# Performance work log

Measured on AMD Instinct MI355X. Metric: run time of the kernel, lower is better.

The kernel has to match this reference:

```python
import jax, jax.numpy as jnp
import numpy as np

N_BINS = 10  # init default of ECELoss


def setup_inputs() -> dict:
    key = jax.random.key(0)
    k1, k2 = jax.random.split(key)
    N, C = 2_000_000, 100
    raw = jax.random.normal(k1, (N, C), dtype=jnp.float32)
    # module computes exp(logits) and expects confidences in (0, 1],
    # so the logits it receives are log-probabilities
    logits = jax.nn.log_softmax(raw, axis=1)
    labels = jax.random.randint(k2, (N,), 0, C, dtype=jnp.int64)
    return {"logits": logits, "labels": labels}


def reference(logits, labels):
    softmaxes = jnp.exp(logits)                       # [N, C]
    confidences = jnp.max(softmaxes, axis=1)          # [N]
    predictions = jnp.argmax(softmaxes, axis=1)       # [N]
    accuracies = (predictions == labels).astype(jnp.float32)

    n = confidences.shape[0]
    # bin i holds conf in (i/n_bins, (i+1)/n_bins]  ->  ceil(conf*n_bins)-1
    bin_idx = jnp.ceil(confidences * N_BINS).astype(jnp.int32) - 1
    # conf <= 0 belongs to no bin (strict lower bound on bin 0); conf > 1
    # already maps to an out-of-range index. Out-of-range ids are dropped
    # by segment_sum.
    bin_idx = jnp.where(confidences <= 0.0, N_BINS, bin_idx)

    ones = jnp.ones_like(confidences)
    counts = jax.ops.segment_sum(ones, bin_idx, num_segments=N_BINS)
    sum_conf = jax.ops.segment_sum(confidences, bin_idx, num_segments=N_BINS)
    sum_acc = jax.ops.segment_sum(accuracies, bin_idx, num_segments=N_BINS)

    prop_in_bin = counts / n
    safe = jnp.maximum(counts, 1.0)
    gap = jnp.abs(sum_conf / safe - sum_acc / safe)
    ece = jnp.sum(jnp.where(counts > 0, gap * prop_in_bin, 0.0))
    return ece.reshape(1)
```

## Files before the change

kernel.cpp:

```cpp
#include <hip/hip_runtime.h>
#include <math.h>

#define NBINS 10
#define MAIN_BLOCKS 2048
#define MAIN_THREADS 256


__global__ void ece_zero_ws(float* ws) {
    int i = threadIdx.x;
    if (i < 3 * NBINS) ws[i] = 0.0f;
}

__global__ __launch_bounds__(MAIN_THREADS) void ece_main(
        const float* __restrict__ logits,
        const int* __restrict__ labels,
        float* __restrict__ ws,
        int N) {
    __shared__ float sbin[3 * NBINS];
    const int tid = threadIdx.x;
    if (tid < 3 * NBINS) sbin[tid] = 0.0f;
    __syncthreads();

    const int lane = tid & 63;
    const int waveInBlock = tid >> 6;
    const int wavesPerBlock = MAIN_THREADS >> 6;
    const long long globalWave = (long long)blockIdx.x * wavesPerBlock + waveInBlock;
    const long long totalWaves = (long long)gridDim.x * wavesPerBlock;

    const int half = lane >> 5;
    const int hlane = lane & 31;

    const long long nPairs = ((long long)N + 1) >> 1;
    const float4* logits4 = (const float4*)logits;

    for (long long p = globalWave; p < nPairs; p += totalWaves) {
        const long long row = 2 * p + half;
        const bool rowValid = (row < (long long)N);

        float m = -INFINITY;
        int midx = 0;
        if (rowValid && hlane < 25) {
            float4 v = logits4[row * 25 + hlane];
            const int e = hlane * 4;
            m = v.x; midx = e;
            if (v.y > m) { m = v.y; midx = e + 1; }
            if (v.z > m) { m = v.z; midx = e + 2; }
            if (v.w > m) { m = v.w; midx = e + 3; }
        }

        #pragma unroll
        for (int off = 16; off >= 1; off >>= 1) {
            float om = __shfl_xor(m, off, 32);
            int   oi = __shfl_xor(midx, off, 32);
            if (om > m || (om == m && oi < midx)) { m = om; midx = oi; }
        }

        if (rowValid && hlane == 0) {
            const float conf = expf(m);
            const int b = (int)ceilf(conf * 10.0f) - 1;
            const float acc = (midx == labels[row]) ? 1.0f : 0.0f;
            if (b >= 0 && b < NBINS) {
                atomicAdd(&sbin[b], 1.0f);
                atomicAdd(&sbin[NBINS + b], conf);
                atomicAdd(&sbin[2 * NBINS + b], acc);
            }
        }
    }

    __syncthreads();
    if (tid < 3 * NBINS) {
        const float v = sbin[tid];
        if (v != 0.0f) atomicAdd(&ws[tid], v);
    }
}

__global__ void ece_final(const float* __restrict__ ws, float* __restrict__ out, int N) {
    if (threadIdx.x == 0 && blockIdx.x == 0) {
        float ece = 0.0f;
        for (int b = 0; b < NBINS; ++b) {
            const float cnt = ws[b];
            if (cnt > 0.0f) {
                const float avg_conf = ws[NBINS + b] / cnt;
                const float avg_acc  = ws[2 * NBINS + b] / cnt;
                ece += fabsf(avg_conf - avg_acc) * (cnt / (float)N);
            }
        }
        out[0] = ece;
    }
}

extern "C" void kernel_launch(void* const* d_in, const int* in_sizes, int n_in,
                              void* d_out, int out_size, void* d_ws, size_t ws_size,
                              hipStream_t stream) {
    const float* logits = (const float*)d_in[0];
    const int*   labels = (const int*)d_in[1];
    float* out = (float*)d_out;
    float* ws  = (float*)d_ws;

    const int N = in_sizes[1];

    ece_zero_ws<<<1, 64, 0, stream>>>(ws);
    ece_main<<<MAIN_BLOCKS, MAIN_THREADS, 0, stream>>>(logits, labels, ws, N);
    ece_final<<<1, 64, 0, stream>>>(ws, out, N);
}
```

Before: 1.040 ms.

## Switch to one thread per row with a full register-held row scan

Each thread now loads an entire 100-float row as 25 float4 values into registers and runs a sequential argmax, replacing the scheme where half-waves split a row and reduced it with shuffles. This removes the shuffle reduction and the idle lanes, and gives each thread many independent loads in flight. The cost is uncoalesced access: adjacent threads read addresses 400 bytes apart. It also uses far more registers, which lowers occupancy, and shared-memory atomics now come from every thread at once and may contend.

```diff
diff --git a/kernel.cpp b/kernel.cpp
--- a/kernel.cpp
+++ b/kernel.cpp
@@ -4,6 +4,7 @@
 #define NBINS 10
 #define MAIN_BLOCKS 2048
 #define MAIN_THREADS 256
+#define NV4 25
 
 
 __global__ void ece_zero_ws(float* ws) {
@@ -21,56 +22,42 @@
     if (tid < 3 * NBINS) sbin[tid] = 0.0f;
     __syncthreads();
 
-    const int lane = tid & 63;
-    const int waveInBlock = tid >> 6;
-    const int wavesPerBlock = MAIN_THREADS >> 6;
-    const long long globalWave = (long long)blockIdx.x * wavesPerBlock + waveInBlock;
-    const long long totalWaves = (long long)gridDim.x * wavesPerBlock;
+    const float4* __restrict__ lg4 = (const float4*)logits;
+    const long long stride = (long long)gridDim.x * MAIN_THREADS;
+    long long row = (long long)blockIdx.x * MAIN_THREADS + tid;
 
-    const int half = lane >> 5;
-    const int hlane = lane & 31;
+    for (; row < (long long)N; row += stride) {
+        const float4* __restrict__ rp = lg4 + row * NV4;
 
-    const long long nPairs = ((long long)N + 1) >> 1;
-    const float4* logits4 = (const float4*)logits;
-
-    for (long long p = globalWave; p < nPairs; p += totalWaves) {
-        const long long row = 2 * p + half;
-        const bool rowValid = (row < (long long)N);
+        float4 v[NV4];
+        #pragma unroll
+        for (int j = 0; j < NV4; ++j) v[j] = rp[j];
 
         float m = -INFINITY;
         int midx = 0;
-        if (rowValid && hlane < 25) {
-            float4 v = logits4[row * 25 + hlane];
-            const int e = hlane * 4;
-            m = v.x; midx = e;
-            if (v.y > m) { m = v.y; midx = e + 1; }
-            if (v.z > m) { m = v.z; midx = e + 2; }
-            if (v.w > m) { m = v.w; midx = e + 3; }
+        #pragma unroll
+        for (int j = 0; j < NV4; ++j) {
+            const int e = 4 * j;
+            if (v[j].x > m) { m = v[j].x; midx = e; }
+            if (v[j].y > m) { m = v[j].y; midx = e + 1; }
+            if (v[j].z > m) { m = v[j].z; midx = e + 2; }
+            if (v[j].w > m) { m = v[j].w; midx = e + 3; }
         }
 
-        #pragma unroll
-        for (int off = 16; off >= 1; off >>= 1) {
-            float om = __shfl_xor(m, off, 32);
-            int   oi = __shfl_xor(midx, off, 32);
-            if (om > m || (om == m && oi < midx)) { m = om; midx = oi; }
-        }
-
-        if (rowValid && hlane == 0) {
-            const float conf = expf(m);
-            const int b = (int)ceilf(conf * 10.0f) - 1;
-            const float acc = (midx == labels[row]) ? 1.0f : 0.0f;
-            if (b >= 0 && b < NBINS) {
-                atomicAdd(&sbin[b], 1.0f);
-                atomicAdd(&sbin[NBINS + b], conf);
-                atomicAdd(&sbin[2 * NBINS + b], acc);
-            }
+        const float conf = expf(m);
+        const int b = (int)ceilf(conf * 10.0f) - 1;
+        const float acc = (midx == labels[row]) ? 1.0f : 0.0f;
+        if (b >= 0 && b < NBINS) {
+            atomicAdd(&sbin[b], 1.0f);
+            atomicAdd(&sbin[NBINS + b], conf);
+            atomicAdd(&sbin[2 * NBINS + b], acc);
         }
     }
 
     __syncthreads();
     if (tid < 3 * NBINS) {
-        const float v = sbin[tid];
-        if (v != 0.0f) atomicAdd(&ws[tid], v);
+        const float s = sbin[tid];
+        if (s != 0.0f) atomicAdd(&ws[tid], s);
     }
 }
 
```

Result: faster. 1.019 ms (-2.0%).
